# Kernel optimization log

Hardware: AMD Instinct MI355X
Metric: run time of the kernel (lower is better)

## Reference

```python
import jax, jax.numpy as jnp
import numpy as np

N = 65536   # total nodes
E = 1048576 # total edges (avg degree 16)
B = 512     # graphs in batch
H = 4       # gat1 heads
C = 64      # per-head channels / GNN_HIDDEN


def segment_softmax(logits, seg, num_segments):
    # numerically stable softmax over segments (PyG softmax semantics, eps=1e-16)
    m = jax.ops.segment_max(logits, seg, num_segments=num_segments)
    m = jnp.where(jnp.isfinite(m), m, 0.0)
    e = jnp.exp(logits - m[seg])
    s = jax.ops.segment_sum(e, seg, num_segments=num_segments)
    return e / (s[seg] + 1e-16)


def gat_conv(x, edge_index, edge_attr, W, att_src, att_dst, We, att_edge, bias, heads, out_ch, concat):
    # PyG GATConv with edge_dim, add_self_loops=False
    n = x.shape[0]
    h = (x @ W).reshape(n, heads, out_ch)                 # (N,H,C)
    src, dst = edge_index[0], edge_index[1]
    a_s = jnp.sum(h * att_src, axis=-1)                   # (N,H)
    a_d = jnp.sum(h * att_dst, axis=-1)                   # (N,H)
    he = (edge_attr @ We).reshape(-1, heads, out_ch)      # (E,H,C)
    a_e = jnp.sum(he * att_edge, axis=-1)                 # (E,H)
    alpha = jax.nn.leaky_relu(a_s[src] + a_d[dst] + a_e, negative_slope=0.2)
    alpha = segment_softmax(alpha, dst, n)                # softmax over incoming edges per dst
    out = jax.ops.segment_sum(h[src] * alpha[..., None], dst, num_segments=n)  # (N,H,C)
    out = out.reshape(n, heads * out_ch) if concat else out.mean(axis=1)
    return out + bias


def setup_inputs() -> dict:
    key = jax.random.key(0)
    ks = jax.random.split(key, 24)
    s = 0.05
    d = {}
    d["global_feat"] = jax.random.normal(ks[0], (B, 512), jnp.float32)
    d["x"] = jax.random.normal(ks[1], (N, 13), jnp.float32)
    d["roi_feats"] = jax.random.normal(ks[2], (N, 256), jnp.float32)
    d["edge_index"] = jax.random.randint(ks[3], (2, E), 0, N)
    d["edge_attr"] = jax.random.normal(ks[4], (E, 5), jnp.float32)
    d["batch_vec"] = jnp.sort(jax.random.randint(ks[5], (N,), 0, B))
    # roi_proj / scene_proj
    d["roi_W"] = jax.random.normal(ks[6], (256, 64), jnp.float32) * s
    d["roi_b"] = jnp.zeros((64,), jnp.float32)
    d["scene_W"] = jax.random.normal(ks[7], (512, 128), jnp.float32) * s
    d["scene_b"] = jnp.zeros((128,), jnp.float32)
    d["g1_W"] = jax.random.normal(ks[8], (77, H * C), jnp.float32) * s
    d["g1_att_src"] = jax.random.normal(ks[9], (H, C), jnp.float32) * s
    d["g1_att_dst"] = jax.random.normal(ks[10], (H, C), jnp.float32) * s
    d["g1_We"] = jax.random.normal(ks[11], (5, H * C), jnp.float32) * s
    d["g1_att_edge"] = jax.random.normal(ks[12], (H, C), jnp.float32) * s
    d["g1_bias"] = jnp.zeros((H * C,), jnp.float32)
    # gat2: 256 -> 64, 1 head
    d["g2_W"] = jax.random.normal(ks[13], (H * C, C), jnp.float32) * s
    d["g2_att_src"] = jax.random.normal(ks[14], (1, C), jnp.float32) * s
    d["g2_att_dst"] = jax.random.normal(ks[15], (1, C), jnp.float32) * s
    d["g2_We"] = jax.random.normal(ks[16], (5, C), jnp.float32) * s
    d["g2_att_edge"] = jax.random.normal(ks[17], (1, C), jnp.float32) * s
    d["g2_bias"] = jnp.zeros((C,), jnp.float32)
    # attention pooling gate + classifier
    d["gate_W"] = jax.random.normal(ks[18], (C, 1), jnp.float32) * s
    d["gate_b"] = jnp.zeros((1,), jnp.float32)
    d["cls1_W"] = jax.random.normal(ks[19], (128 + C, 64), jnp.float32) * s
    d["cls1_b"] = jnp.zeros((64,), jnp.float32)
    d["cls2_W"] = jax.random.normal(ks[20], (64, 3), jnp.float32) * s
    d["cls2_b"] = jnp.zeros((3,), jnp.float32)
    return d


def reference(global_feat, x, roi_feats, edge_index, edge_attr, batch_vec,
              roi_W, roi_b, scene_W, scene_b,
              g1_W, g1_att_src, g1_att_dst, g1_We, g1_att_edge, g1_bias,
              g2_W, g2_att_src, g2_att_dst, g2_We, g2_att_edge, g2_bias,
              gate_W, gate_b, cls1_W, cls1_b, cls2_W, cls2_b):
    scene = global_feat @ scene_W + scene_b                       # (B,128)
    vis = jax.nn.relu(roi_feats @ roi_W + roi_b)                  # (N,64)
    h = jnp.concatenate([x, vis], axis=-1)                        # (N,77)
    h = jax.nn.relu(gat_conv(h, edge_index, edge_attr, g1_W, g1_att_src, g1_att_dst, g1_We, g1_att_edge, g1_bias, H, C, True))
    h = gat_conv(h, edge_index, edge_attr, g2_W, g2_att_src, g2_att_dst, g2_We, g2_att_edge, g2_bias, 1, C, False)  # (N,64)
    # GlobalAttention pooling
    gate = segment_softmax((h @ gate_W + gate_b)[:, 0], batch_vec, B)
    rel = jax.ops.segment_sum(gate[:, None] * h, batch_vec, num_segments=B)  # (B,64)
    comb = jnp.concatenate([scene, rel], axis=-1)                 # (B,192)
    hid = jax.nn.relu(comb @ cls1_W + cls1_b)                     # dropout off (eval)
    return hid @ cls2_W + cls2_b                                  # (B,3)
```

## Files before the change

### kernel.cpp

```cpp
#include <hip/hip_runtime.h>

#define N_NODES 65536
#define N_EDGES 1048576
#define NB      512

typedef unsigned short u16;
typedef unsigned int   u32;
typedef unsigned long long u64;

__device__ __forceinline__ float bf2f(u16 u) { return __uint_as_float(((u32)u) << 16); }
__device__ __forceinline__ float lo16(u32 u) { return __uint_as_float(u << 16); }
__device__ __forceinline__ float hi16(u32 u) { return __uint_as_float(u & 0xffff0000u); }
__device__ __forceinline__ u16 f2bf(float f) {
    u32 u = __float_as_uint(f);
    u32 r = (u + 0x7fffu + ((u >> 16) & 1u)) >> 16;
    return (u16)r;
}
__device__ __forceinline__ float wsum(float v) {
    for (int o = 32; o; o >>= 1) v += __shfl_xor(v, o, 64);
    return v;
}
__device__ __forceinline__ float wmax(float v) {
    for (int o = 32; o; o >>= 1) v = fmaxf(v, __shfl_xor(v, o, 64));
    return v;
}

__global__ void k_prep(const float* g1We, const float* g1ae, const float* g2We, const float* g2ae,
                       float* M1, float* M2) {
    int t = threadIdx.x;
    if (t < 20) {
        int j = t >> 2, h = t & 3;
        float s = 0.f;
        for (int c = 0; c < 64; c++) s += g1We[j * 256 + h * 64 + c] * g1ae[h * 64 + c];
        M1[t] = s;
    } else if (t < 25) {
        int j = t - 20;
        float s = 0.f;
        for (int c = 0; c < 64; c++) s += g2We[j * 64 + c] * g2ae[c];
        M2[j] = s;
    }
}

__global__ __launch_bounds__(256) void k_scene(const float* __restrict__ gf, const float* __restrict__ W,
                                               const float* __restrict__ bias, float* __restrict__ scene) {
    int idx = blockIdx.x * 256 + threadIdx.x;
    int b = idx >> 7, j = idx & 127;
    float acc = 0.f;
    for (int k = 0; k < 512; k++) acc += gf[b * 512 + k] * W[k * 128 + j];
    scene[idx] = acc + bias[j];
}

__global__ __launch_bounds__(256) void k_hist(const int* ei, int* cnt) {
    int e = blockIdx.x * 256 + threadIdx.x;
    atomicAdd(&cnt[ei[N_EDGES + e]], 1);
}

__global__ __launch_bounds__(256) void k_scan_blk(const int* __restrict__ cnt, int* __restrict__ pre,
                                                  int* __restrict__ bsum) {
    __shared__ int sd[256];
    int t = threadIdx.x, b = blockIdx.x;
    int base = b * 1024 + t * 4;
    int4 c = *(const int4*)(cnt + base);
    int s = c.x + c.y + c.z + c.w;
    sd[t] = s;
    __syncthreads();
    for (int off = 1; off < 256; off <<= 1) {
        int v = (t >= off) ? sd[t - off] : 0;
        __syncthreads();
        sd[t] += v;
        __syncthreads();
    }
    int excl = sd[t] - s;
    int4 p;
    p.x = excl;
    p.y = excl + c.x;
    p.z = excl + c.x + c.y;
    p.w = excl + c.x + c.y + c.z;
    *(int4*)(pre + base) = p;
    if (t == 255) bsum[b] = sd[255];
}

__global__ __launch_bounds__(64) void k_scan_top(int* bsum) {
    int t = threadIdx.x;
    int v = bsum[t];
    int inc = v;
    for (int off = 1; off < 64; off <<= 1) {
        int u = __shfl_up(inc, off, 64);
        if (t >= off) inc += u;
    }
    bsum[t] = inc - v;
}

__global__ __launch_bounds__(256) void k_scan_fix(const int* __restrict__ pre, const int* __restrict__ bsum,
                                                  int* __restrict__ row_ptr, int* __restrict__ coarse_cur) {
    int i = blockIdx.x * 256 + threadIdx.x;
    int v = pre[i] + bsum[i >> 10];
    row_ptr[i] = v;
    if ((i & 255) == 0) coarse_cur[i >> 8] = v;
    if (i == 0) row_ptr[N_NODES] = N_EDGES;
}

__global__ __launch_bounds__(256) void k_bucket(const int* __restrict__ ei, int* coarse_cur,
                                                u32* __restrict__ bpack, int* __restrict__ bsrc) {
    __shared__ u32 stageP[4096];
    __shared__ int stageS[4096];
    __shared__ int bcnt[256], bscan[256], boff[256], gbase[256];
    int t = threadIdx.x;
    int e0 = blockIdx.x * 4096;
    bcnt[t] = 0;
    __syncthreads();
    int dreg[16], sreg[16];
    for (int it = 0; it < 16; it++) {
        int e = e0 + it * 256 + t;
        int dd = ei[N_EDGES + e];
        dreg[it] = dd;
        sreg[it] = ei[e];
        atomicAdd(&bcnt[dd >> 8], 1);
    }
    __syncthreads();
    int v = bcnt[t];
    bscan[t] = v;
    __syncthreads();
    for (int off = 1; off < 256; off <<= 1) {
        int u = (t >= off) ? bscan[t - off] : 0;
        __syncthreads();
        bscan[t] += u;
        __syncthreads();
    }
    boff[t] = bscan[t] - v;
    gbase[t] = v ? atomicAdd(&coarse_cur[t], v) : 0;
    __syncthreads();
    for (int it = 0; it < 16; it++) {
        int e = e0 + it * 256 + t;
        int b = dreg[it] >> 8;
        int pos = atomicAdd(&boff[b], 1);
        stageP[pos] = ((u32)e << 12) | (u32)(dreg[it] & 255);
        stageS[pos] = sreg[it];
    }
    __syncthreads();
    for (int idx = t; idx < 4096; idx += 256) {
        int lo = 0, hi = 255;
        while (lo < hi) { int mid = (lo + hi) >> 1; if (bscan[mid] > idx) hi = mid; else lo = mid + 1; }
        int b = lo;
        int g = gbase[b] + (idx - (bscan[b] - bcnt[b]));
        bpack[g] = stageP[idx];
        bsrc[g] = stageS[idx];
    }
}

__global__ __launch_bounds__(256) void k_sortb(const u32* __restrict__ bpack, const int* __restrict__ bsrc,
                                               const int* __restrict__ row_ptr,
                                               int* __restrict__ eord, int* __restrict__ ssrc) {
    __shared__ int cur[256];
    int t = threadIdx.x, b = blockIdx.x;
    int nbase = b * 256;
    cur[t] = row_ptr[nbase + t];
    __syncthreads();
    int beg = row_ptr[nbase];
    int end = row_ptr[nbase + 256];
    for (int i = beg + t; i < end; i += 256) {
        u32 wd = bpack[i];
        int src = bsrc[i];
        int d8 = wd & 255;
        int pos = atomicAdd(&cur[d8], 1);
        eord[pos] = (int)(wd >> 12);
        ssrc[pos] = src;
    }
}

__global__ __launch_bounds__(256) void k_payload(const int* __restrict__ eord, const float* __restrict__ ea,
                                                 const float* __restrict__ M1, const float* __restrict__ M2,
                                                 float* __restrict__ a1es, float* __restrict__ a2es) {
    int pos = blockIdx.x * 256 + threadIdx.x;
    int e = eord[pos];
    float v[5];
    for (int j = 0; j < 5; j++) v[j] = ea[(size_t)e * 5 + j];
    float4 o;
    o.x = v[0]*M1[0]  + v[1]*M1[4]  + v[2]*M1[8]  + v[3]*M1[12] + v[4]*M1[16];
    o.y = v[0]*M1[1]  + v[1]*M1[5]  + v[2]*M1[9]  + v[3]*M1[13] + v[4]*M1[17];
    o.z = v[0]*M1[2]  + v[1]*M1[6]  + v[2]*M1[10] + v[3]*M1[14] + v[4]*M1[18];
    o.w = v[0]*M1[3]  + v[1]*M1[7]  + v[2]*M1[11] + v[3]*M1[15] + v[4]*M1[19];
    *(float4*)(a1es + (size_t)pos * 4) = o;
    a2es[pos] = v[0]*M2[0] + v[1]*M2[1] + v[2]*M2[2] + v[3]*M2[3] + v[4]*M2[4];
}

__global__ __launch_bounds__(256) void k_vis(const float* __restrict__ A, const float* __restrict__ W,
                                             const float* __restrict__ bias, float* __restrict__ out) {
    __shared__ float At[64][68];
    __shared__ float Wl[64][68];
    int t = threadIdx.x;
    int n0 = blockIdx.x * 64;
    int cg = t & 15, rg = t >> 4;
    int sr = t >> 2, scs = (t & 3) * 16;
    float acc[4][4];
    for (int i = 0; i < 4; i++) for (int j = 0; j < 4; j++) acc[i][j] = 0.f;
    for (int kc = 0; kc < 4; kc++) {
        __syncthreads();
        const float* ap = A + (size_t)(n0 + sr) * 256 + kc * 64 + scs;
        float4 q0 = *(const float4*)ap, q1 = *(const float4*)(ap + 4);
        float4 q2 = *(const float4*)(ap + 8), q3 = *(const float4*)(ap + 12);
        At[scs + 0][sr] = q0.x;  At[scs + 1][sr] = q0.y;  At[scs + 2][sr] = q0.z;  At[scs + 3][sr] = q0.w;
        At[scs + 4][sr] = q1.x;  At[scs + 5][sr] = q1.y;  At[scs + 6][sr] = q1.z;  At[scs + 7][sr] = q1.w;
        At[scs + 8][sr] = q2.x;  At[scs + 9][sr] = q2.y;  At[scs + 10][sr] = q2.z; At[scs + 11][sr] = q2.w;
        At[scs + 12][sr] = q3.x; At[scs + 13][sr] = q3.y; At[scs + 14][sr] = q3.z; At[scs + 15][sr] = q3.w;
        const float* wp = W + (size_t)(kc * 64 + sr) * 64 + scs;
        *(float4*)&Wl[sr][scs + 0]  = *(const float4*)wp;
        *(float4*)&Wl[sr][scs + 4]  = *(const float4*)(wp + 4);
        *(float4*)&Wl[sr][scs + 8]  = *(const float4*)(wp + 8);
        *(float4*)&Wl[sr][scs + 12] = *(const float4*)(wp + 12);
        __syncthreads();
        for (int k = 0; k < 64; k++) {
            float4 a4 = *(const float4*)&At[k][rg * 4];
            float4 w4 = *(const float4*)&Wl[k][cg * 4];
            acc[0][0] += a4.x * w4.x; acc[0][1] += a4.x * w4.y; acc[0][2] += a4.x * w4.z; acc[0][3] += a4.x * w4.w;
            acc[1][0] += a4.y * w4.x; acc[1][1] += a4.y * w4.y; acc[1][2] += a4.y * w4.z; acc[1][3] += a4.y * w4.w;
            acc[2][0] += a4.z * w4.x; acc[2][1] += a4.z * w4.y; acc[2][2] += a4.z * w4.z; acc[2][3] += a4.z * w4.w;
            acc[3][0] += a4.w * w4.x; acc[3][1] += a4.w * w4.y; acc[3][2] += a4.w * w4.z; acc[3][3] += a4.w * w4.w;
        }
    }
    float4 bb = *(const float4*)(bias + cg * 4);
    for (int i = 0; i < 4; i++) {
        float4 o;
        o.x = fmaxf(acc[i][0] + bb.x, 0.f);
        o.y = fmaxf(acc[i][1] + bb.y, 0.f);
        o.z = fmaxf(acc[i][2] + bb.z, 0.f);
        o.w = fmaxf(acc[i][3] + bb.w, 0.f);
        *(float4*)(out + (size_t)(n0 + rg * 4 + i) * 64 + cg * 4) = o;
    }
}

__global__ __launch_bounds__(256) void k_h2(const u16* __restrict__ A, const float* __restrict__ W,
                                            const float* __restrict__ as_, const float* __restrict__ ad_,
                                            u16* __restrict__ out, float* __restrict__ a2s,
                                            float* __restrict__ a2d) {
    __shared__ float At[64][68];
    __shared__ float Wl[64][68];
    int t = threadIdx.x;
    int n0 = blockIdx.x * 64;
    int cg = t & 15, rg = t >> 4;
    int sr = t >> 2, scs = (t & 3) * 16;
    float acc[4][4];
    for (int i = 0; i < 4; i++) for (int j = 0; j < 4; j++) acc[i][j] = 0.f;
    for (int kc = 0; kc < 4; kc++) {
        __syncthreads();
        const u16* ap = A + (size_t)(n0 + sr) * 256 + kc * 64 + scs;
        uint4 u0 = *(const uint4*)ap;
        uint4 u1 = *(const uint4*)(ap + 8);
        At[scs + 0][sr] = lo16(u0.x);  At[scs + 1][sr] = hi16(u0.x);
        At[scs + 2][sr] = lo16(u0.y);  At[scs + 3][sr] = hi16(u0.y);
        At[scs + 4][sr] = lo16(u0.z);  At[scs + 5][sr] = hi16(u0.z);
        At[scs + 6][sr] = lo16(u0.w);  At[scs + 7][sr] = hi16(u0.w);
        At[scs + 8][sr] = lo16(u1.x);  At[scs + 9][sr] = hi16(u1.x);
        At[scs + 10][sr] = lo16(u1.y); At[scs + 11][sr] = hi16(u1.y);
        At[scs + 12][sr] = lo16(u1.z); At[scs + 13][sr] = hi16(u1.z);
        At[scs + 14][sr] = lo16(u1.w); At[scs + 15][sr] = hi16(u1.w);
        const float* wp = W + (size_t)(kc * 64 + sr) * 64 + scs;
        *(float4*)&Wl[sr][scs + 0]  = *(const float4*)wp;
        *(float4*)&Wl[sr][scs + 4]  = *(const float4*)(wp + 4);
        *(float4*)&Wl[sr][scs + 8]  = *(const float4*)(wp + 8);
        *(float4*)&Wl[sr][scs + 12] = *(const float4*)(wp + 12);
        __syncthreads();
        for (int k = 0; k < 64; k++) {
            float4 a4 = *(const float4*)&At[k][rg * 4];
            float4 w4 = *(const float4*)&Wl[k][cg * 4];
            acc[0][0] += a4.x * w4.x; acc[0][1] += a4.x * w4.y; acc[0][2] += a4.x * w4.z; acc[0][3] += a4.x * w4.w;
            acc[1][0] += a4.y * w4.x; acc[1][1] += a4.y * w4.y; acc[1][2] += a4.y * w4.z; acc[1][3] += a4.y * w4.w;
            acc[2][0] += a4.z * w4.x; acc[2][1] += a4.z * w4.y; acc[2][2] += a4.z * w4.z; acc[2][3] += a4.z * w4.w;
            acc[3][0] += a4.w * w4.x; acc[3][1] += a4.w * w4.y; acc[3][2] += a4.w * w4.z; acc[3][3] += a4.w * w4.w;
        }
    }
    u32* outu = (u32*)out;
    for (int i = 0; i < 4; i++) {
        uint2 pk;
        pk.x = (u32)f2bf(acc[i][0]) | ((u32)f2bf(acc[i][1]) << 16);
        pk.y = (u32)f2bf(acc[i][2]) | ((u32)f2bf(acc[i][3]) << 16);
        *(uint2*)(outu + (size_t)(n0 + rg * 4 + i) * 32 + cg * 2) = pk;
    }
    float4 as4 = *(const float4*)(as_ + cg * 4);
    float4 ad4 = *(const float4*)(ad_ + cg * 4);
    #pragma unroll
    for (int i = 0; i < 4; i++) {
        float ps = acc[i][0] * as4.x + acc[i][1] * as4.y + acc[i][2] * as4.z + acc[i][3] * as4.w;
        float pd = acc[i][0] * ad4.x + acc[i][1] * ad4.y + acc[i][2] * ad4.z + acc[i][3] * ad4.w;
        for (int o = 1; o < 16; o <<= 1) { ps += __shfl_xor(ps, o, 64); pd += __shfl_xor(pd, o, 64); }
        if (cg == 0) {
            a2s[n0 + rg * 4 + i] = ps;
            a2d[n0 + rg * 4 + i] = pd;
        }
    }
}

__global__ __launch_bounds__(256) void k_h1(const float* __restrict__ x, const float* __restrict__ vis,
                                            const float* __restrict__ g1W,
                                            const float* __restrict__ as_, const float* __restrict__ ad_,
                                            u16* __restrict__ h1, float* __restrict__ a1s,
                                            float* __restrict__ a1d) {
    __shared__ float At[77][36];
    __shared__ float Wl[77][132];
    int t = threadIdx.x, ch = blockIdx.y;
    int n0 = blockIdx.x * 32;
    int cg = t & 31, rg = t >> 5;
    for (int idx = t; idx < 9856; idx += 256) {
        int k = idx >> 7, c = idx & 127;
        Wl[k][c] = g1W[(size_t)k * 256 + ch * 128 + c];
    }
    for (int idx = t; idx < 2464; idx += 256) {
        int r = idx / 77, k = idx - r * 77;
        At[k][r] = (k < 13) ? x[(size_t)(n0 + r) * 13 + k] : vis[(size_t)(n0 + r) * 64 + (k - 13)];
    }
    __syncthreads();
    float acc[4][4];
    for (int i = 0; i < 4; i++) for (int j = 0; j < 4; j++) acc[i][j] = 0.f;
    for (int k = 0; k < 77; k++) {
        float4 a4 = *(const float4*)&At[k][rg * 4];
        float4 w4 = *(const float4*)&Wl[k][cg * 4];
        acc[0][0] += a4.x * w4.x; acc[0][1] += a4.x * w4.y; acc[0][2] += a4.x * w4.z; acc[0][3] += a4.x * w4.w;
        acc[1][0] += a4.y * w4.x; acc[1][1] += a4.y * w4.y; acc[1][2] += a4.y * w4.z; acc[1][3] += a4.y * w4.w;
        acc[2][0] += a4.z * w4.x; acc[2][1] += a4.z * w4.y; acc[2][2] += a4.z * w4.z; acc[2][3] += a4.z * w4.w;
        acc[3][0] += a4.w * w4.x; acc[3][1] += a4.w * w4.y; acc[3][2] += a4.w * w4.z; acc[3][3] += a4.w * w4.w;
    }
    for (int i = 0; i < 4; i++) {
        uint2 pk;
        pk.x = (u32)f2bf(acc[i][0]) | ((u32)f2bf(acc[i][1]) << 16);
        pk.y = (u32)f2bf(acc[i][2]) | ((u32)f2bf(acc[i][3]) << 16);
        *(uint2*)(h1 + (size_t)(n0 + rg * 4 + i) * 256 + ch * 128 + cg * 4) = pk;
    }
    int gh = ch * 2 + (cg >> 4);
    int co = (cg & 15) * 4;
    float4 as4 = *(const float4*)(as_ + gh * 64 + co);
    float4 ad4 = *(const float4*)(ad_ + gh * 64 + co);
    #pragma unroll
    for (int i = 0; i < 4; i++) {
        float ps = acc[i][0] * as4.x + acc[i][1] * as4.y + acc[i][2] * as4.z + acc[i][3] * as4.w;
        float pd = acc[i][0] * ad4.x + acc[i][1] * ad4.y + acc[i][2] * ad4.z + acc[i][3] * ad4.w;
        for (int o = 1; o < 16; o <<= 1) { ps += __shfl_xor(ps, o, 64); pd += __shfl_xor(pd, o, 64); }
        if ((cg & 15) == 0) {
            int n = n0 + rg * 4 + i;
            a1s[n * 4 + gh] = ps;
            a1d[n * 4 + gh] = pd;
        }
    }
}

__global__ __launch_bounds__(256) void k_soft1(const int* __restrict__ row_ptr, const int* __restrict__ ssrc,
                                               const float* __restrict__ a1s, const float* __restrict__ a1d,
                                               const float* __restrict__ a1es, float* __restrict__ w1,
                                               float2* __restrict__ minv1) {
    int t = threadIdx.x;
    int wv = t >> 6, L = t & 63;
    int n = blockIdx.x * 4 + wv;
    int h = L >> 4, j = L & 15;
    int beg = row_ptr[n], deg = row_ptr[n + 1] - beg;
    if (deg == 0) return;
    float adn = a1d[n * 4 + h];
    float m = -3.0e38f, s = 0.f;
    for (int i = j; i < deg; i += 16) {
        int pos = beg + i;
        float l = a1s[ssrc[pos] * 4 + h] + adn + a1es[(size_t)pos * 4 + h];
        l = (l > 0.f) ? l : 0.2f * l;
        w1[(size_t)pos * 4 + h] = l;
        if (l > m) { s = s * __expf(m - l) + 1.f; m = l; }
        else       { s += __expf(l - m); }
    }
    for (int o = 1; o < 16; o <<= 1) {
        float mo = __shfl_xor(m, o, 64), so = __shfl_xor(s, o, 64);
        float M = fmaxf(m, mo);
        s = s * __expf(m - M) + so * __expf(mo - M);
        m = M;
    }
    if (j == 0) minv1[n * 4 + h] = make_float2(m, 1.f / (s + 1e-16f));
}

__global__ __launch_bounds__(256) void k_gath1(const int* __restrict__ row_ptr, const int* __restrict__ ssrc,
                                               const float* __restrict__ w1, const float2* __restrict__ minv1,
                                               const u16* __restrict__ h1,
                                               const float* __restrict__ bias, u16* __restrict__ out1) {
    int t = threadIdx.x;
    int wv = t >> 6, L = t & 63;
    int n = blockIdx.x * 4 + wv;
    int beg = row_ptr[n], deg = row_ptr[n + 1] - beg;
    int halfE = L >> 5;
    int L32 = L & 31;
    int hd = L32 >> 3;
    float2 mi = (deg > 0) ? minv1[n * 4 + hd] : make_float2(0.f, 0.f);
    float acc[8];
    #pragma unroll
    for (int j = 0; j < 8; j++) acc[j] = 0.f;
    int last = beg + deg - 1;
    for (int i = 0; i < deg; i += 8) {
        int iA = i + halfE, iB = i + 2 + halfE, iC = i + 4 + halfE, iD = i + 6 + halfE;
        bool vA = iA < deg, vB = iB < deg, vC = iC < deg, vD = iD < deg;
        int cA = vA ? beg + iA : last, cB = vB ? beg + iB : last;
        int cC = vC ? beg + iC : last, cD = vD ? beg + iD : last;
        int sA = ssrc[cA], sB = ssrc[cB], sC = ssrc[cC], sD = ssrc[cD];
        float lA = w1[(size_t)cA * 4 + hd];
        float lB = w1[(size_t)cB * 4 + hd];
        float lC = w1[(size_t)cC * 4 + hd];
        float lD = w1[(size_t)cD * 4 + hd];
        float wA = vA ? __expf(lA - mi.x) * mi.y : 0.f;
        float wB = vB ? __expf(lB - mi.x) * mi.y : 0.f;
        float wC = vC ? __expf(lC - mi.x) * mi.y : 0.f;
        float wD = vD ? __expf(lD - mi.x) * mi.y : 0.f;
        uint4 uA = *((const uint4*)(h1 + (size_t)sA * 256) + L32);
        uint4 uB = *((const uint4*)(h1 + (size_t)sB * 256) + L32);
        uint4 uC = *((const uint4*)(h1 + (size_t)sC * 256) + L32);
        uint4 uD = *((const uint4*)(h1 + (size_t)sD * 256) + L32);
        acc[0] += wA * lo16(uA.x) + wB * lo16(uB.x) + wC * lo16(uC.x) + wD * lo16(uD.x);
        acc[1] += wA * hi16(uA.x) + wB * hi16(uB.x) + wC * hi16(uC.x) + wD * hi16(uD.x);
        acc[2] += wA * lo16(uA.y) + wB * lo16(uB.y) + wC * lo16(uC.y) + wD * lo16(uD.y);
        acc[3] += wA * hi16(uA.y) + wB * hi16(uB.y) + wC * hi16(uC.y) + wD * hi16(uD.y);
        acc[4] += wA * lo16(uA.z) + wB * lo16(uB.z) + wC * lo16(uC.z) + wD * lo16(uD.z);
        acc[5] += wA * hi16(uA.z) + wB * hi16(uB.z) + wC * hi16(uC.z) + wD * hi16(uD.z);
        acc[6] += wA * lo16(uA.w) + wB * lo16(uB.w) + wC * lo16(uC.w) + wD * lo16(uD.w);
        acc[7] += wA * hi16(uA.w) + wB * hi16(uB.w) + wC * hi16(uC.w) + wD * hi16(uD.w);
    }
    #pragma unroll
    for (int j = 0; j < 8; j++) acc[j] += __shfl_xor(acc[j], 32, 64);
    if (halfE == 0) {
        float4 b0 = *(const float4*)(bias + 8 * L32);
        float4 b1 = *(const float4*)(bias + 8 * L32 + 4);
        uint4 pk;
        pk.x = (u32)f2bf(fmaxf(acc[0] + b0.x, 0.f)) | ((u32)f2bf(fmaxf(acc[1] + b0.y, 0.f)) << 16);
        pk.y = (u32)f2bf(fmaxf(acc[2] + b0.z, 0.f)) | ((u32)f2bf(fmaxf(acc[3] + b0.w, 0.f)) << 16);
        pk.z = (u32)f2bf(fmaxf(acc[4] + b1.x, 0.f)) | ((u32)f2bf(fmaxf(acc[5] + b1.y, 0.f)) << 16);
        pk.w = (u32)f2bf(fmaxf(acc[6] + b1.z, 0.f)) | ((u32)f2bf(fmaxf(acc[7] + b1.w, 0.f)) << 16);
        *((uint4*)(out1 + (size_t)n * 256) + L32) = pk;
    }
}

__global__ __launch_bounds__(256) void k_soft2(const int* __restrict__ row_ptr, const int* __restrict__ ssrc,
                                               const float* __restrict__ a2s, const float* __restrict__ a2d,
                                               const float* __restrict__ a2es, float* __restrict__ w2,
                                               float2* __restrict__ minv2) {
    int t = threadIdx.x;
    int wv = t >> 6, L = t & 63;
    int g = L >> 4, j = L & 15;
    int n = blockIdx.x * 16 + wv * 4 + g;
    int beg = row_ptr[n], deg = row_ptr[n + 1] - beg;
    if (deg == 0) return;
    float adn = a2d[n];
    float m = -3.0e38f, s = 0.f;
    for (int i = j; i < deg; i += 16) {
        int pos = beg + i;
        float l = a2s[ssrc[pos]] + adn + a2es[pos];
        l = (l > 0.f) ? l : 0.2f * l;
        w2[pos] = l;
        if (l > m) { s = s * __expf(m - l) + 1.f; m = l; }
        else       { s += __expf(l - m); }
    }
    for (int o = 1; o < 16; o <<= 1) {
        float mo = __shfl_xor(m, o, 64), so = __shfl_xor(s, o, 64);
        float M = fmaxf(m, mo);
        s = s * __expf(m - M) + so * __expf(mo - M);
        m = M;
    }
    if (j == 0) minv2[n] = make_float2(m, 1.f / (s + 1e-16f));
}

__global__ __launch_bounds__(256) void k_gath2(const int* __restrict__ row_ptr, const int* __restrict__ ssrc,
                                               const float* __restrict__ w2, const float2* __restrict__ minv2,
                                               const u16* __restrict__ h2b,
                                               const float* __restrict__ bias, float* __restrict__ hfin) {
    int t = threadIdx.x;
    int wv = t >> 6, L = t & 63;
    int n = blockIdx.x * 4 + wv;
    int beg = row_ptr[n], deg = row_ptr[n + 1] - beg;
    int halfE = L >> 5;
    int L32 = L & 31;
    float2 mi = (deg > 0) ? minv2[n] : make_float2(0.f, 0.f);
    float a0 = 0.f, a1v = 0.f;
    int last = beg + deg - 1;
    const u32* h2u = (const u32*)h2b;
    for (int i = 0; i < deg; i += 8) {
        int iA = i + halfE, iB = i + 2 + halfE, iC = i + 4 + halfE, iD = i + 6 + halfE;
        bool vA = iA < deg, vB = iB < deg, vC = iC < deg, vD = iD < deg;
        int cA = vA ? beg + iA : last, cB = vB ? beg + iB : last;
        int cC = vC ? beg + iC : last, cD = vD ? beg + iD : last;
        int sA = ssrc[cA], sB = ssrc[cB], sC = ssrc[cC], sD = ssrc[cD];
        float lA = w2[cA], lB = w2[cB], lC = w2[cC], lD = w2[cD];
        float wA = vA ? __expf(lA - mi.x) * mi.y : 0.f;
        float wB = vB ? __expf(lB - mi.x) * mi.y : 0.f;
        float wC = vC ? __expf(lC - mi.x) * mi.y : 0.f;
        float wD = vD ? __expf(lD - mi.x) * mi.y : 0.f;
        u32 uA = h2u[(size_t)sA * 32 + L32];
        u32 uB = h2u[(size_t)sB * 32 + L32];
        u32 uC = h2u[(size_t)sC * 32 + L32];
        u32 uD = h2u[(size_t)sD * 32 + L32];
        a0  += wA * lo16(uA) + wB * lo16(uB) + wC * lo16(uC) + wD * lo16(uD);
        a1v += wA * hi16(uA) + wB * hi16(uB) + wC * hi16(uC) + wD * hi16(uD);
    }
    a0  += __shfl_xor(a0, 32, 64);
    a1v += __shfl_xor(a1v, 32, 64);
    if (halfE == 0) {
        float2 o;
        o.x = a0  + bias[2 * L32];
        o.y = a1v + bias[2 * L32 + 1];
        *(float2*)(hfin + (size_t)n * 64 + 2 * L32) = o;
    }
}

__global__ __launch_bounds__(64) void k_pool(const int* __restrict__ bvec, const float* __restrict__ hf,
                                             const float* gateW, const float* gateb,
                                             const float* __restrict__ scene,
                                             const float* c1W, const float* c1b,
                                             const float* c2W, const float* c2b,
                                             float* __restrict__ outp) {
    int b = blockIdx.x, lane = threadIdx.x;
    __shared__ float gwl[64], se[64], comb[192], hid[64];
    gwl[lane] = gateW[lane];
    __syncthreads();
    int s0, s1;
    { int lo = 0, hi = N_NODES; while (lo < hi) { int mid = (lo + hi) >> 1; if (bvec[mid] < b) lo = mid + 1; else hi = mid; } s0 = lo; }
    { int lo = 0, hi = N_NODES; while (lo < hi) { int mid = (lo + hi) >> 1; if (bvec[mid] < b + 1) lo = mid + 1; else hi = mid; } s1 = lo; }
    float gb = gateb[0];
    float m = -3.0e38f, ssum = 0.f, acc = 0.f;
    for (int cs = s0; cs < s1; cs += 64) {
        int cnt = min(64, s1 - cs);
        float l = -3.0e38f;
        if (lane < cnt) {
            int n = cs + lane;
            float d = 0.f;
            for (int i = 0; i < 64; i++) d += hf[(size_t)n * 64 + i] * gwl[i];
            l = d + gb;
        }
        float cm = wmax(l);
        float newm = fmaxf(m, cm);
        float rsc = __expf(m - newm);
        float e = (lane < cnt) ? __expf(l - newm) : 0.f;
        float es = wsum(e);
        ssum = ssum * rsc + es;
        se[lane] = e;
        __syncthreads();
        float a2 = 0.f;
        for (int i = 0; i < cnt; i++) a2 += se[i] * hf[(size_t)(cs + i) * 64 + lane];
        acc = acc * rsc + a2;
        __syncthreads();
        m = newm;
    }
    float rel = acc / (ssum + 1e-16f);
    comb[lane] = scene[b * 128 + lane];
    comb[64 + lane] = scene[b * 128 + 64 + lane];
    comb[128 + lane] = rel;
    __syncthreads();
    float hj = 0.f;
    for (int k = 0; k < 192; k++) hj += comb[k] * c1W[k * 64 + lane];
    hj += c1b[lane];
    hid[lane] = fmaxf(hj, 0.f);
    __syncthreads();
    if (lane < 3) {
        float o = 0.f;
        for (int k = 0; k < 64; k++) o += hid[k] * c2W[k * 3 + lane];
        o += c2b[lane];
        outp[b * 3 + lane] = o;
    }
}

extern "C" void kernel_launch(void* const* d_in, const int* in_sizes, int n_in,
                              void* d_out, int out_size, void* d_ws, size_t ws_size,
                              hipStream_t stream) {
    (void)in_sizes; (void)n_in; (void)out_size; (void)ws_size;
    const float* gf     = (const float*)d_in[0];
    const float* x      = (const float*)d_in[1];
    const float* roi    = (const float*)d_in[2];
    const int*   ei     = (const int*)d_in[3];
    const float* ea     = (const float*)d_in[4];
    const int*   bvec   = (const int*)d_in[5];
    const float* roiW   = (const float*)d_in[6];
    const float* roib   = (const float*)d_in[7];
    const float* sceneW = (const float*)d_in[8];
    const float* sceneb = (const float*)d_in[9];
    const float* g1W    = (const float*)d_in[10];
    const float* g1as   = (const float*)d_in[11];
    const float* g1ad   = (const float*)d_in[12];
    const float* g1We   = (const float*)d_in[13];
    const float* g1ae   = (const float*)d_in[14];
    const float* g1b    = (const float*)d_in[15];
    const float* g2W    = (const float*)d_in[16];
    const float* g2as   = (const float*)d_in[17];
    const float* g2ad   = (const float*)d_in[18];
    const float* g2We   = (const float*)d_in[19];
    const float* g2ae   = (const float*)d_in[20];
    const float* g2b    = (const float*)d_in[21];
    const float* gateW  = (const float*)d_in[22];
    const float* gateb  = (const float*)d_in[23];
    const float* c1W    = (const float*)d_in[24];
    const float* c1b    = (const float*)d_in[25];
    const float* c2W    = (const float*)d_in[26];
    const float* c2b    = (const float*)d_in[27];

    char* w = (char*)d_ws;
    size_t o = 0;
    auto nxt = [&](size_t bytes) -> char* {
        char* p = w + o;
        o += (bytes + 255) & ~(size_t)255;
        return p;
    };
    float* scene  = (float*)nxt((size_t)NB * 128 * 4);
    float* M1     = (float*)nxt(80);
    float* M2     = (float*)nxt(32);
    int* cnt      = (int*)nxt((size_t)N_NODES * 4);
    int* pre      = (int*)nxt((size_t)N_NODES * 4);
    int* bsum     = (int*)nxt(64 * 4);
    int* row_ptr  = (int*)nxt((size_t)(N_NODES + 1) * 4);
    int* coarse   = (int*)nxt(256 * 4);
    u32* bpack    = (u32*)nxt((size_t)N_EDGES * 4);
    int* bsrc     = (int*)nxt((size_t)N_EDGES * 4);
    int* eord     = (int*)nxt((size_t)N_EDGES * 4);
    int* ssrc     = (int*)nxt((size_t)N_EDGES * 4);
    float* a1es   = (float*)nxt((size_t)N_EDGES * 16);
    float* a2es   = (float*)nxt((size_t)N_EDGES * 4);
    float* visbuf = (float*)nxt((size_t)N_NODES * 64 * 4);
    u16* h1       = (u16*)nxt((size_t)N_NODES * 256 * 2);
    u16* out1     = (u16*)nxt((size_t)N_NODES * 256 * 2);
    float* w1buf  = (float*)nxt((size_t)N_EDGES * 16);
    float* hfin   = (float*)nxt((size_t)N_NODES * 64 * 4);
    float* a1s    = (float*)nxt((size_t)N_NODES * 16);
    float* a1d    = (float*)nxt((size_t)N_NODES * 16);
    float* a2s    = (float*)nxt((size_t)N_NODES * 4);
    float* a2d    = (float*)nxt((size_t)N_NODES * 4);
    float2* minv1 = (float2*)nxt((size_t)N_NODES * 4 * 8);
    float2* minv2 = (float2*)nxt((size_t)N_NODES * 8);

    float* vis = visbuf;
    float* w2  = visbuf;
    float* w1  = w1buf;
    u16*   h2b = (u16*)w1buf;

    hipMemsetAsync(cnt, 0, (size_t)N_NODES * 4, stream);
    k_prep<<<1, 32, 0, stream>>>(g1We, g1ae, g2We, g2ae, M1, M2);
    k_scene<<<(NB * 128) / 256, 256, 0, stream>>>(gf, sceneW, sceneb, scene);
    k_hist<<<N_EDGES / 256, 256, 0, stream>>>(ei, cnt);
    k_scan_blk<<<64, 256, 0, stream>>>(cnt, pre, bsum);
    k_scan_top<<<1, 64, 0, stream>>>(bsum);
    k_scan_fix<<<N_NODES / 256, 256, 0, stream>>>(pre, bsum, row_ptr, coarse);
    k_bucket<<<256, 256, 0, stream>>>(ei, coarse, bpack, bsrc);
    k_sortb<<<256, 256, 0, stream>>>(bpack, bsrc, row_ptr, eord, ssrc);
    k_payload<<<N_EDGES / 256, 256, 0, stream>>>(eord, ea, M1, M2, a1es, a2es);
    k_vis<<<N_NODES / 64, 256, 0, stream>>>(roi, roiW, roib, vis);
    k_h1<<<dim3(N_NODES / 32, 2), 256, 0, stream>>>(x, vis, g1W, g1as, g1ad, h1, a1s, a1d);
    k_soft1<<<N_NODES / 4, 256, 0, stream>>>(row_ptr, ssrc, a1s, a1d, a1es, w1, minv1);
    k_gath1<<<N_NODES / 4, 256, 0, stream>>>(row_ptr, ssrc, w1, minv1, h1, g1b, out1);
    k_h2<<<N_NODES / 64, 256, 0, stream>>>(out1, g2W, g2as, g2ad, h2b, a2s, a2d);
    k_soft2<<<N_NODES / 16, 256, 0, stream>>>(row_ptr, ssrc, a2s, a2d, a2es, w2, minv2);
    k_gath2<<<N_NODES / 4, 256, 0, stream>>>(row_ptr, ssrc, w2, minv2, h2b, g2b, hfin);
    k_pool<<<NB, 64, 0, stream>>>(bvec, hfin, gateW, gateb, scene, c1W, c1b, c2W, c2b, (float*)d_out);
}
```

Measured before the change: 612.9 us.

## Port roi projection and GAT1 linear to bf16 MFMA with pre-transposed weights

Rewrites k_vis and k_h1 to use MFMA 16x16x32 bf16 instructions in place of fp32 FMA loops. Small prep kernels transpose and convert roi_W and g1_W to bf16, with g1_W's K reordered to match a vis-then-x layout padded to 96. The vis intermediate is now stored as bf16, which halves its traffic. This cuts ALU time on two dense GEMMs but adds bf16 rounding of inputs and two tiny extra launches.

Result: faster. 550.8 us (-10.1%).

```diff
diff --git a/kernel.cpp b/kernel.cpp
--- a/kernel.cpp
+++ b/kernel.cpp
@@ -7,6 +7,9 @@
 typedef unsigned short u16;
 typedef unsigned int   u32;
 typedef unsigned long long u64;
+
+typedef __attribute__((ext_vector_type(8))) short bf16x8;
+typedef __attribute__((ext_vector_type(4))) float f32x4;
 
 __device__ __forceinline__ float bf2f(u16 u) { return __uint_as_float(((u32)u) << 16); }
 __device__ __forceinline__ float lo16(u32 u) { return __uint_as_float(u << 16); }
@@ -15,6 +18,9 @@
     u32 u = __float_as_uint(f);
     u32 r = (u + 0x7fffu + ((u >> 16) & 1u)) >> 16;
     return (u16)r;
+}
+__device__ __forceinline__ u32 pk2(float a, float b) {
+    return (u32)f2bf(a) | ((u32)f2bf(b) << 16);
 }
 __device__ __forceinline__ float wsum(float v) {
     for (int o = 32; o; o >>= 1) v += __shfl_xor(v, o, 64);
@@ -39,6 +45,23 @@
         for (int c = 0; c < 64; c++) s += g2We[j * 64 + c] * g2ae[c];
         M2[j] = s;
     }
+}
+
+__global__ void k_wt1(const float* __restrict__ g1W, u16* __restrict__ Wt) {
+    int c = blockIdx.x;
+    int k = threadIdx.x;
+    float v = 0.f;
+    if (k < 77) {
+        int ko = (k < 64) ? (13 + k) : (k - 64);
+        v = g1W[(size_t)ko * 256 + c];
+    }
+    Wt[(size_t)c * 96 + k] = f2bf(v);
+}
+
+__global__ void k_wtv(const float* __restrict__ roiW, u16* __restrict__ Wt) {
+    int c = blockIdx.x;
+    int k = threadIdx.x;
+    Wt[(size_t)c * 256 + k] = f2bf(roiW[(size_t)k * 64 + c]);
 }
 
 __global__ __launch_bounds__(256) void k_scene(const float* __restrict__ gf, const float* __restrict__ W,
@@ -184,48 +207,119 @@
     a2es[pos] = v[0]*M2[0] + v[1]*M2[1] + v[2]*M2[2] + v[3]*M2[3] + v[4]*M2[4];
 }
 
-__global__ __launch_bounds__(256) void k_vis(const float* __restrict__ A, const float* __restrict__ W,
-                                             const float* __restrict__ bias, float* __restrict__ out) {
-    __shared__ float At[64][68];
-    __shared__ float Wl[64][68];
-    int t = threadIdx.x;
+__global__ __launch_bounds__(256) void k_vis(const float* __restrict__ roi, const u16* __restrict__ Wt,
+                                             const float* __restrict__ bias, u16* __restrict__ out) {
+    __shared__ u16 At[64][264];
+    int t = threadIdx.x;
+    int w = t >> 6, l = t & 63, lo = l & 15, hi = l >> 4;
     int n0 = blockIdx.x * 64;
-    int cg = t & 15, rg = t >> 4;
-    int sr = t >> 2, scs = (t & 3) * 16;
-    float acc[4][4];
-    for (int i = 0; i < 4; i++) for (int j = 0; j < 4; j++) acc[i][j] = 0.f;
-    for (int kc = 0; kc < 4; kc++) {
-        __syncthreads();
-        const float* ap = A + (size_t)(n0 + sr) * 256 + kc * 64 + scs;
-        float4 q0 = *(const float4*)ap, q1 = *(const float4*)(ap + 4);
-        float4 q2 = *(const float4*)(ap + 8), q3 = *(const float4*)(ap + 12);
-        At[scs + 0][sr] = q0.x;  At[scs + 1][sr] = q0.y;  At[scs + 2][sr] = q0.z;  At[scs + 3][sr] = q0.w;
-        At[scs + 4][sr] = q1.x;  At[scs + 5][sr] = q1.y;  At[scs + 6][sr] = q1.z;  At[scs + 7][sr] = q1.w;
-        At[scs + 8][sr] = q2.x;  At[scs + 9][sr] = q2.y;  At[scs + 10][sr] = q2.z; At[scs + 11][sr] = q2.w;
-        At[scs + 12][sr] = q3.x; At[scs + 13][sr] = q3.y; At[scs + 14][sr] = q3.z; At[scs + 15][sr] = q3.w;
-        const float* wp = W + (size_t)(kc * 64 + sr) * 64 + scs;
-        *(float4*)&Wl[sr][scs + 0]  = *(const float4*)wp;
-        *(float4*)&Wl[sr][scs + 4]  = *(const float4*)(wp + 4);
-        *(float4*)&Wl[sr][scs + 8]  = *(const float4*)(wp + 8);
-        *(float4*)&Wl[sr][scs + 12] = *(const float4*)(wp + 12);
-        __syncthreads();
-        for (int k = 0; k < 64; k++) {
-            float4 a4 = *(const float4*)&At[k][rg * 4];
-            float4 w4 = *(const float4*)&Wl[k][cg * 4];
-            acc[0][0] += a4.x * w4.x; acc[0][1] += a4.x * w4.y; acc[0][2] += a4.x * w4.z; acc[0][3] += a4.x * w4.w;
-            acc[1][0] += a4.y * w4.x; acc[1][1] += a4.y * w4.y; acc[1][2] += a4.y * w4.z; acc[1][3] += a4.y * w4.w;
-            acc[2][0] += a4.z * w4.x; acc[2][1] += a4.z * w4.y; acc[2][2] += a4.z * w4.z; acc[2][3] += a4.z * w4.w;
-            acc[3][0] += a4.w * w4.x; acc[3][1] += a4.w * w4.y; acc[3][2] += a4.w * w4.z; acc[3][3] += a4.w * w4.w;
-        }
-    }
-    float4 bb = *(const float4*)(bias + cg * 4);
-    for (int i = 0; i < 4; i++) {
-        float4 o;
-        o.x = fmaxf(acc[i][0] + bb.x, 0.f);
-        o.y = fmaxf(acc[i][1] + bb.y, 0.f);
-        o.z = fmaxf(acc[i][2] + bb.z, 0.f);
-        o.w = fmaxf(acc[i][3] + bb.w, 0.f);
-        *(float4*)(out + (size_t)(n0 + rg * 4 + i) * 64 + cg * 4) = o;
+    int r = t >> 2, sub = t & 3;
+    const float* rp = roi + (size_t)(n0 + r) * 256 + sub * 4;
+    #pragma unroll
+    for (int q = 0; q < 16; q++) {
+        float4 v = *(const float4*)(rp + q * 16);
+        uint2 p;
+        p.x = pk2(v.x, v.y);
+        p.y = pk2(v.z, v.w);
+        *(uint2*)&At[r][q * 16 + sub * 4] = p;
+    }
+    float bb[4][4];
+    #pragma unroll
+    for (int cb = 0; cb < 4; cb++)
+        #pragma unroll
+        for (int rg = 0; rg < 4; rg++) bb[cb][rg] = bias[cb * 16 + hi * 4 + rg];
+    __syncthreads();
+    f32x4 acc[4];
+    #pragma unroll
+    for (int cb = 0; cb < 4; cb++) acc[cb] = (f32x4){0.f, 0.f, 0.f, 0.f};
+    #pragma unroll
+    for (int ks = 0; ks < 8; ks++) {
+        bf16x8 af = *(const bf16x8*)(&At[w * 16 + lo][ks * 32 + hi * 8]);
+        #pragma unroll
+        for (int cb = 0; cb < 4; cb++) {
+            bf16x8 wf = *(const bf16x8*)(Wt + (size_t)(cb * 16 + lo) * 256 + ks * 32 + hi * 8);
+            acc[cb] = __builtin_amdgcn_mfma_f32_16x16x32_bf16(wf, af, acc[cb], 0, 0, 0);
+        }
+    }
+    int nrow = n0 + w * 16 + lo;
+    #pragma unroll
+    for (int cb = 0; cb < 4; cb++) {
+        uint2 p;
+        p.x = pk2(fmaxf(acc[cb][0] + bb[cb][0], 0.f), fmaxf(acc[cb][1] + bb[cb][1], 0.f));
+        p.y = pk2(fmaxf(acc[cb][2] + bb[cb][2], 0.f), fmaxf(acc[cb][3] + bb[cb][3], 0.f));
+        *(uint2*)(out + (size_t)nrow * 64 + cb * 16 + hi * 4) = p;
+    }
+}
+
+__global__ __launch_bounds__(256) void k_h1(const float* __restrict__ x, const u16* __restrict__ vis,
+                                            const u16* __restrict__ Wt,
+                                            const float* __restrict__ as_, const float* __restrict__ ad_,
+                                            u16* __restrict__ h1, float* __restrict__ a1s,
+                                            float* __restrict__ a1d) {
+    __shared__ u16 At[64][104];
+    int t = threadIdx.x;
+    int w = t >> 6, l = t & 63, lo = l & 15, hi = l >> 4;
+    int n0 = blockIdx.x * 64;
+    int r = t >> 2, sub = t & 3;
+    {
+        const uint4* vp = (const uint4*)(vis + (size_t)(n0 + r) * 64 + sub * 16);
+        uint4 v0 = vp[0], v1 = vp[1];
+        *(uint4*)&At[r][sub * 16] = v0;
+        *(uint4*)&At[r][sub * 16 + 8] = v1;
+        if (sub == 0) {
+            const float* xp = x + (size_t)(n0 + r) * 13;
+            #pragma unroll
+            for (int j = 0; j < 13; j++) At[r][64 + j] = f2bf(xp[j]);
+        } else if (sub == 1) {
+            #pragma unroll
+            for (int j = 77; j < 96; j++) At[r][j] = 0;
+        }
+    }
+    bf16x8 wf[4][3];
+    float asv[4][4], adv[4][4];
+    #pragma unroll
+    for (int cb = 0; cb < 4; cb++) {
+        #pragma unroll
+        for (int ks = 0; ks < 3; ks++)
+            wf[cb][ks] = *(const bf16x8*)(Wt + (size_t)(w * 64 + cb * 16 + lo) * 96 + ks * 32 + hi * 8);
+        #pragma unroll
+        for (int rg = 0; rg < 4; rg++) {
+            asv[cb][rg] = as_[w * 64 + cb * 16 + hi * 4 + rg];
+            adv[cb][rg] = ad_[w * 64 + cb * 16 + hi * 4 + rg];
+        }
+    }
+    __syncthreads();
+    #pragma unroll
+    for (int nb = 0; nb < 4; nb++) {
+        f32x4 acc[4];
+        #pragma unroll
+        for (int cb = 0; cb < 4; cb++) acc[cb] = (f32x4){0.f, 0.f, 0.f, 0.f};
+        #pragma unroll
+        for (int ks = 0; ks < 3; ks++) {
+            bf16x8 af = *(const bf16x8*)(&At[nb * 16 + lo][ks * 32 + hi * 8]);
+            #pragma unroll
+            for (int cb = 0; cb < 4; cb++)
+                acc[cb] = __builtin_amdgcn_mfma_f32_16x16x32_bf16(wf[cb][ks], af, acc[cb], 0, 0, 0);
+        }
+        int nrow = n0 + nb * 16 + lo;
+        float ps = 0.f, pd = 0.f;
+        #pragma unroll
+        for (int cb = 0; cb < 4; cb++) {
+            uint2 p;
+            p.x = pk2(acc[cb][0], acc[cb][1]);
+            p.y = pk2(acc[cb][2], acc[cb][3]);
+            *(uint2*)(h1 + (size_t)nrow * 256 + w * 64 + cb * 16 + hi * 4) = p;
+            ps += acc[cb][0] * asv[cb][0] + acc[cb][1] * asv[cb][1]
+                + acc[cb][2] * asv[cb][2] + acc[cb][3] * asv[cb][3];
+            pd += acc[cb][0] * adv[cb][0] + acc[cb][1] * adv[cb][1]
+                + acc[cb][2] * adv[cb][2] + acc[cb][3] * adv[cb][3];
+        }
+        ps += __shfl_xor(ps, 16, 64); ps += __shfl_xor(ps, 32, 64);
+        pd += __shfl_xor(pd, 16, 64); pd += __shfl_xor(pd, 32, 64);
+        if (hi == 0) {
+            a1s[nrow * 4 + w] = ps;
+            a1d[nrow * 4 + w] = pd;
+        }
     }
 }
 
@@ -286,58 +380,6 @@
         if (cg == 0) {
             a2s[n0 + rg * 4 + i] = ps;
             a2d[n0 + rg * 4 + i] = pd;
-        }
-    }
-}
-
-__global__ __launch_bounds__(256) void k_h1(const float* __restrict__ x, const float* __restrict__ vis,
-                                            const float* __restrict__ g1W,
-                                            const float* __restrict__ as_, const float* __restrict__ ad_,
-                                            u16* __restrict__ h1, float* __restrict__ a1s,
-                                            float* __restrict__ a1d) {
-    __shared__ float At[77][36];
-    __shared__ float Wl[77][132];
-    int t = threadIdx.x, ch = blockIdx.y;
-    int n0 = blockIdx.x * 32;
-    int cg = t & 31, rg = t >> 5;
-    for (int idx = t; idx < 9856; idx += 256) {
-        int k = idx >> 7, c = idx & 127;
-        Wl[k][c] = g1W[(size_t)k * 256 + ch * 128 + c];
-    }
-    for (int idx = t; idx < 2464; idx += 256) {
-        int r = idx / 77, k = idx - r * 77;
-        At[k][r] = (k < 13) ? x[(size_t)(n0 + r) * 13 + k] : vis[(size_t)(n0 + r) * 64 + (k - 13)];
-    }
-    __syncthreads();
-    float acc[4][4];
-    for (int i = 0; i < 4; i++) for (int j = 0; j < 4; j++) acc[i][j] = 0.f;
-    for (int k = 0; k < 77; k++) {
-        float4 a4 = *(const float4*)&At[k][rg * 4];
-        float4 w4 = *(const float4*)&Wl[k][cg * 4];
-        acc[0][0] += a4.x * w4.x; acc[0][1] += a4.x * w4.y; acc[0][2] += a4.x * w4.z; acc[0][3] += a4.x * w4.w;
-        acc[1][0] += a4.y * w4.x; acc[1][1] += a4.y * w4.y; acc[1][2] += a4.y * w4.z; acc[1][3] += a4.y * w4.w;
-        acc[2][0] += a4.z * w4.x; acc[2][1] += a4.z * w4.y; acc[2][2] += a4.z * w4.z; acc[2][3] += a4.z * w4.w;
-        acc[3][0] += a4.w * w4.x; acc[3][1] += a4.w * w4.y; acc[3][2] += a4.w * w4.z; acc[3][3] += a4.w * w4.w;
-    }
-    for (int i = 0; i < 4; i++) {
-        uint2 pk;
-        pk.x = (u32)f2bf(acc[i][0]) | ((u32)f2bf(acc[i][1]) << 16);
-        pk.y = (u32)f2bf(acc[i][2]) | ((u32)f2bf(acc[i][3]) << 16);
-        *(uint2*)(h1 + (size_t)(n0 + rg * 4 + i) * 256 + ch * 128 + cg * 4) = pk;
-    }
-    int gh = ch * 2 + (cg >> 4);
-    int co = (cg & 15) * 4;
-    float4 as4 = *(const float4*)(as_ + gh * 64 + co);
-    float4 ad4 = *(const float4*)(ad_ + gh * 64 + co);
-    #pragma unroll
-    for (int i = 0; i < 4; i++) {
-        float ps = acc[i][0] * as4.x + acc[i][1] * as4.y + acc[i][2] * as4.z + acc[i][3] * as4.w;
-        float pd = acc[i][0] * ad4.x + acc[i][1] * ad4.y + acc[i][2] * ad4.z + acc[i][3] * ad4.w;
-        for (int o = 1; o < 16; o <<= 1) { ps += __shfl_xor(ps, o, 64); pd += __shfl_xor(pd, o, 64); }
-        if ((cg & 15) == 0) {
-            int n = n0 + rg * 4 + i;
-            a1s[n * 4 + gh] = ps;
-            a1d[n * 4 + gh] = pd;
         }
     }
 }
@@ -598,6 +640,8 @@
     float* scene  = (float*)nxt((size_t)NB * 128 * 4);
     float* M1     = (float*)nxt(80);
     float* M2     = (float*)nxt(32);
+    u16* g1Wt     = (u16*)nxt((size_t)256 * 96 * 2);
+    u16* roiWt    = (u16*)nxt((size_t)64 * 256 * 2);
     int* cnt      = (int*)nxt((size_t)N_NODES * 4);
     int* pre      = (int*)nxt((size_t)N_NODES * 4);
     int* bsum     = (int*)nxt(64 * 4);
@@ -621,13 +665,15 @@
     float2* minv1 = (float2*)nxt((size_t)N_NODES * 4 * 8);
     float2* minv2 = (float2*)nxt((size_t)N_NODES * 8);
 
-    float* vis = visbuf;
-    float* w2  = visbuf;
-    float* w1  = w1buf;
+    u16* visb = (u16*)visbuf;
+    float* w2 = visbuf;
+    float* w1 = w1buf;
     u16*   h2b = (u16*)w1buf;
 
     hipMemsetAsync(cnt, 0, (size_t)N_NODES * 4, stream);
     k_prep<<<1, 32, 0, stream>>>(g1We, g1ae, g2We, g2ae, M1, M2);
+    k_wt1<<<256, 96, 0, stream>>>(g1W, g1Wt);
+    k_wtv<<<64, 256, 0, stream>>>(roiW, roiWt);
     k_scene<<<(NB * 128) / 256, 256, 0, stream>>>(gf, sceneW, sceneb, scene);
     k_hist<<<N_EDGES / 256, 256, 0, stream>>>(ei, cnt);
     k_scan_blk<<<64, 256, 0, stream>>>(cnt, pre, bsum);
@@ -636,8 +682,8 @@
     k_bucket<<<256, 256, 0, stream>>>(ei, coarse, bpack, bsrc);
     k_sortb<<<256, 256, 0, stream>>>(bpack, bsrc, row_ptr, eord, ssrc);
     k_payload<<<N_EDGES / 256, 256, 0, stream>>>(eord, ea, M1, M2, a1es, a2es);
-    k_vis<<<N_NODES / 64, 256, 0, stream>>>(roi, roiW, roib, vis);
-    k_h1<<<dim3(N_NODES / 32, 2), 256, 0, stream>>>(x, vis, g1W, g1as, g1ad, h1, a1s, a1d);
+    k_vis<<<N_NODES / 64, 256, 0, stream>>>(roi, roiWt, roib, visb);
+    k_h1<<<N_NODES / 64, 256, 0, stream>>>(x, visb, g1Wt, g1as, g1ad, h1, a1s, a1d);
     k_soft1<<<N_NODES / 4, 256, 0, stream>>>(row_ptr, ssrc, a1s, a1d, a1es, w1, minv1);
     k_gath1<<<N_NODES / 4, 256, 0, stream>>>(row_ptr, ssrc, w1, minv1, h1, g1b, out1);
     k_h2<<<N_NODES / 64, 256, 0, stream>>>(out1, g2W, g2as, g2ad, h2b, a2s, a2d);
```
